# Optimization experiments

Hardware: AMD Instinct MI355X
Metric: run time of the kernel (lower is better)

Reference implementation:

```python
import jax, jax.numpy as jnp
import numpy as np

N_NODES = 50000
N_EDGES = 800000
D = 64          # node_in_feats == out_feats
N_STEPS = 3


def setup_inputs() -> dict:
    key = jax.random.key(0)
    ks = jax.random.split(key, 9)
    s = 1.0 / np.sqrt(D)
    return {
        "node_in": jax.random.normal(ks[0], (N_NODES, D), jnp.float32),
        # edge-type-0 linear (DGL GatedGraphConv self.linears[0])
        "W": jax.random.uniform(ks[1], (D, D), jnp.float32, -s, s),
        "b": jax.random.uniform(ks[2], (D,), jnp.float32, -s, s),
        # GRUCell params (torch layout: rows = [r, z, n] blocks)
        "Wih": jax.random.uniform(ks[3], (3 * D, D), jnp.float32, -s, s),
        "Whh": jax.random.uniform(ks[4], (3 * D, D), jnp.float32, -s, s),
        "bih": jax.random.uniform(ks[5], (3 * D,), jnp.float32, -s, s),
        "bhh": jax.random.uniform(ks[6], (3 * D,), jnp.float32, -s, s),
        "src": jax.random.randint(ks[7], (N_EDGES,), 0, N_NODES, jnp.int32),
        "dst": jax.random.randint(ks[8], (N_EDGES,), 0, N_NODES, jnp.int32),
    }


def _gru_cell(x, h, Wih, Whh, bih, bhh):
    gi = x @ Wih.T + bih   # [N, 3D]
    gh = h @ Whh.T + bhh   # [N, 3D]
    i_r, i_z, i_n = jnp.split(gi, 3, axis=-1)
    h_r, h_z, h_n = jnp.split(gh, 3, axis=-1)
    r = jax.nn.sigmoid(i_r + h_r)
    z = jax.nn.sigmoid(i_z + h_z)
    n = jnp.tanh(i_n + r * h_n)
    return (1.0 - z) * n + z * h


def reference(node_in, W, b, Wih, Whh, bih, bhh, src, dst):
    # DGL GatedGraphConv, n_steps=3, n_etypes=1. node_in_feats == out_feats,
    # so no zero-padding needed. The wrapper's tanh/dropout result is
    # discarded (h is overwritten by the second conv1 call), so the module
    # output is exactly one GatedGraphConv forward.
    h = node_in
    for _ in range(N_STEPS):
        wh = h @ W.T + b                                   # per-node transform; edge msg = wh[src]
        msg = wh[src]                                      # [E, D] gather
        a = jax.ops.segment_sum(msg, dst, num_segments=N_NODES)  # scatter-sum aggregation
        h = _gru_cell(a, h, Wih, Whh, bih, bhh)
    return h
```

## Files before the change

### kernel.cpp

```cpp
#include <hip/hip_runtime.h>

#define D 64
#define EXS 388
#define SGS 72
#define CHUNK 8192
#define PTH 512
#define MAXB 4096

typedef __bf16 bf16x8 __attribute__((ext_vector_type(8)));
typedef float f32x4 __attribute__((ext_vector_type(4)));

union U16 { uint4 u; bf16x8 b; };

__device__ __forceinline__ unsigned short f2bf(float f) {
    unsigned u = __float_as_uint(f);
    u += 0x7fff + ((u >> 16) & 1);
    return (unsigned short)(u >> 16);
}
__device__ __forceinline__ float bf2f(unsigned short s) {
    return __uint_as_float(((unsigned)s) << 16);
}


__global__ __launch_bounds__(256) void setup_kernel(const float* __restrict__ in,
                                                    unsigned short* __restrict__ hb0,
                                                    unsigned short* __restrict__ hb1,
                                                    const float* __restrict__ W,
                                                    const float* __restrict__ Wih,
                                                    const float* __restrict__ Whh,
                                                    const float* __restrict__ b,
                                                    unsigned short* __restrict__ Bpack,
                                                    float* __restrict__ cvec,
                                                    int* __restrict__ gcnt,
                                                    int n4, int nCvt, int N, int NBUK) {
    if ((int)blockIdx.x < nCvt) {
        int i = blockIdx.x * 256 + threadIdx.x;
        if (i < n4) {
            float4 v = ((const float4*)in)[i];
            ushort4 o;
            o.x = f2bf(v.x); o.y = f2bf(v.y); o.z = f2bf(v.z); o.w = f2bf(v.w);
            ((ushort4*)hb0)[i] = o;
        }
        if (blockIdx.x == 0) {
            if (threadIdx.x < 16) {
                ((ushort4*)(hb0 + (size_t)N * D))[threadIdx.x] = (ushort4){0, 0, 0, 0};
                ((ushort4*)(hb1 + (size_t)N * D))[threadIdx.x] = (ushort4){0, 0, 0, 0};
            }
            for (int j = threadIdx.x; j < NBUK; j += 256) gcnt[j] = 0;
        }
        return;
    }
    if (threadIdx.x >= 128) return;
    int blk = blockIdx.x - nCvt;
    int g = blk >> 2, t = blk & 3;
    int ks = threadIdx.x >> 6, lane = threadIdx.x & 63;
    int col = (g % 3) * 64 + t * 16 + (lane & 15);
    int kbase = ks * 32 + ((lane >> 4) & 3) * 8;
    size_t base = ((size_t)(blk * 2 + ks) * 64 + lane) * 8;
#pragma unroll
    for (int j = 0; j < 8; ++j) {
        int k = kbase + j;
        float v;
        if (g < 3) {
            v = 0.f;
#pragma unroll
            for (int m = 0; m < D; ++m) v += Wih[col * D + m] * W[m * D + k];
        } else {
            v = Whh[col * D + k];
        }
        Bpack[base + j] = f2bf(v);
    }
    if (g < 3 && ks == 0 && ((lane >> 4) & 3) == 0) {
        float acc = 0.f;
#pragma unroll
        for (int k = 0; k < D; ++k) acc += Wih[col * D + k] * b[k];
        cvec[col] = acc;
    }
}


__global__ __launch_bounds__(256) void count_kernel(const int* __restrict__ dst,
                                                    int* __restrict__ gcnt,
                                                    int E, int NBUK) {
    __shared__ int h[512];
    int g = blockIdx.x;
    for (int i = threadIdx.x; i < NBUK; i += 256) h[i] = 0;
    __syncthreads();
    int beg = g * CHUNK;
    int end = min(beg + CHUNK, E);
    for (int i = beg + threadIdx.x; i < end; i += 256)
        atomicAdd(&h[dst[i] >> 7], 1);
    __syncthreads();
    for (int i = threadIdx.x; i < NBUK; i += 256)
        if (h[i]) atomicAdd(&gcnt[i], h[i]);
}

__global__ __launch_bounds__(512) void bscan_kernel(const int* __restrict__ gcnt,
                                                    int* __restrict__ bucket_off,
                                                    int* __restrict__ gcursor,
                                                    int NBUK, int E) {
    __shared__ int scn[512];
    int t = threadIdx.x;
    int own = (t < NBUK) ? gcnt[t] : 0;
    scn[t] = own;
    __syncthreads();
    for (int off = 1; off < 512; off <<= 1) {
        int cur = scn[t];
        int add = (t >= off) ? scn[t - off] : 0;
        __syncthreads();
        scn[t] = cur + add;
        __syncthreads();
    }
    if (t < NBUK) {
        int excl = scn[t] - own;
        bucket_off[t] = excl;
        gcursor[t] = excl;
    }
    if (t == 0) bucket_off[NBUK] = E;
}

__global__ __launch_bounds__(PTH) void partition_kernel(const int* __restrict__ src,
                                                        const int* __restrict__ dst,
                                                        int* __restrict__ gcursor,
                                                        unsigned* __restrict__ pairs,
                                                        int E, int NBUK) {
    __shared__ unsigned pl[CHUNK];
    __shared__ unsigned short bk[CHUNK];
    __shared__ int hist[512];
    __shared__ int scn[512];
    __shared__ int goff[512];
    int g = blockIdx.x;
    int t = threadIdx.x;
    int beg = g * CHUNK;
    int end = min(beg + CHUNK, E);
    int m = end - beg;
    hist[t] = 0;
    __syncthreads();
    for (int i = t; i < m; i += PTH)
        atomicAdd(&hist[dst[beg + i] >> 7], 1);
    __syncthreads();
    int own = hist[t];
    scn[t] = own;
    __syncthreads();
    for (int off = 1; off < 512; off <<= 1) {
        int cur = scn[t];
        int add = (t >= off) ? scn[t - off] : 0;
        __syncthreads();
        scn[t] = cur + add;
        __syncthreads();
    }
    int excl = scn[t] - own;
    hist[t] = excl;
    if (t < NBUK) {
        int gbase = own ? atomicAdd(&gcursor[t], own) : 0;
        goff[t] = gbase - excl;
    }
    __syncthreads();
    for (int i = t; i < m; i += PTH) {
        int d = dst[beg + i];
        int s = src[beg + i];
        int b = d >> 7;
        int pos = atomicAdd(&hist[b], 1);
        pl[pos] = ((unsigned)s << 7) | (unsigned)(d & 127);
        bk[pos] = (unsigned short)b;
    }
    __syncthreads();
    for (int i = t; i < m; i += PTH)
        pairs[goff[bk[i]] + i] = pl[i];
}

__global__ __launch_bounds__(256) void bucket_sort_kernel(const unsigned* __restrict__ pairs,
                                                          const int* __restrict__ bucket_off,
                                                          int* __restrict__ srcs_sorted,
                                                          int* __restrict__ row_off,
                                                          int E, int NBUK, int N) {
    __shared__ unsigned pl[MAXB];
    __shared__ int srcl[MAXB];
    __shared__ int cnt[128];
    __shared__ int sc[128];
    __shared__ int cur2[128];
    int b = blockIdx.x;
    int t = threadIdx.x;
    int beg = bucket_off[b];
    int end = bucket_off[b + 1];
    int m = end - beg;
    if (m > MAXB) m = MAXB;
    if (t < 128) cnt[t] = 0;
    __syncthreads();
    for (int i = t; i < m; i += 256) {
        unsigned p = pairs[beg + i];
        pl[i] = p;
        atomicAdd(&cnt[p & 127], 1);
    }
    __syncthreads();
    int vt = 0;
    if (t < 128) { vt = cnt[t]; sc[t] = vt; }
    __syncthreads();
    for (int off = 1; off < 128; off <<= 1) {
        int v2 = 0;
        if (t < 128) { v2 = sc[t] + ((t >= off) ? sc[t - off] : 0); }
        __syncthreads();
        if (t < 128) sc[t] = v2;
        __syncthreads();
    }
    int excl = (t < 128) ? (sc[t] - vt) : 0;
    if (t < 128) {
        int gid = b * 128 + t;
        if (gid < N) row_off[gid] = beg + excl;
        cur2[t] = excl;
    }
    if (b == NBUK - 1 && t == 0) row_off[N] = E;
    __syncthreads();
    for (int i = t; i < m; i += 256) {
        unsigned p = pl[i];
        int r = atomicAdd(&cur2[p & 127], 1);
        srcl[r] = (int)(p >> 7);
    }
    __syncthreads();
    for (int i = t; i < m; i += 256) srcs_sorted[beg + i] = srcl[i];
}


__global__ __launch_bounds__(512) void fused2_kernel(const unsigned short* __restrict__ hb_in,
                                                     unsigned short* __restrict__ hb_out,
                                                     float* __restrict__ Fout, int writeF32,
                                                     const unsigned short* __restrict__ Bpack,
                                                     const float* __restrict__ cvec,
                                                     const float* __restrict__ bih,
                                                     const float* __restrict__ bhh,
                                                     const int* __restrict__ row_off,
                                                     const int* __restrict__ srcs,
                                                     int N) {
    __shared__ unsigned short sg[16 * SGS];
    __shared__ float ex[16 * EXS];
    int tid = threadIdx.x;
    int g = tid >> 6;
    int lane = tid & 63;
    int base = blockIdx.x * 16;

    {
        int es = lane >> 3;
        int fo = lane & 7;
        int nlA = g, nlB = g + 8;
        int nodeA = base + nlA, nodeB = base + nlB;
        int begA = 0, endA = 0, begB = 0, endB = 0;
        if (nodeA < N) { begA = row_off[nodeA]; endA = row_off[nodeA + 1]; }
        if (nodeB < N) { begB = row_off[nodeB]; endB = row_off[nodeB + 1]; }

        int sA[4], sB[4];
#pragma unroll
        for (int j = 0; j < 4; ++j) {
            int eA = begA + 8 * j + es;
            int eB = begB + 8 * j + es;
            sA[j] = (eA < endA) ? srcs[eA] : N;
            sB[j] = (eB < endB) ? srcs[eB] : N;
        }
        uint4 dA[4], dB[4];
#pragma unroll
        for (int j = 0; j < 4; ++j) dA[j] = *(const uint4*)(hb_in + (size_t)sA[j] * D + fo * 8);
#pragma unroll
        for (int j = 0; j < 4; ++j) dB[j] = *(const uint4*)(hb_in + (size_t)sB[j] * D + fo * 8);

        float accA[8], accB[8];
#pragma unroll
        for (int j = 0; j < 8; ++j) { accA[j] = 0.f; accB[j] = 0.f; }
#pragma unroll
        for (int j = 0; j < 4; ++j) {
            unsigned ua[4] = {dA[j].x, dA[j].y, dA[j].z, dA[j].w};
            unsigned ub[4] = {dB[j].x, dB[j].y, dB[j].z, dB[j].w};
#pragma unroll
            for (int k = 0; k < 4; ++k) {
                accA[2 * k]     += bf2f((unsigned short)(ua[k] & 0xffff));
                accA[2 * k + 1] += bf2f((unsigned short)(ua[k] >> 16));
                accB[2 * k]     += bf2f((unsigned short)(ub[k] & 0xffff));
                accB[2 * k + 1] += bf2f((unsigned short)(ub[k] >> 16));
            }
        }
        for (int i = begA + 32; i < endA; i += 8) {
            int e = i + es;
            int s = (e < endA) ? srcs[e] : N;
            uint4 dd = *(const uint4*)(hb_in + (size_t)s * D + fo * 8);
            unsigned uu[4] = {dd.x, dd.y, dd.z, dd.w};
#pragma unroll
            for (int k = 0; k < 4; ++k) {
                accA[2 * k]     += bf2f((unsigned short)(uu[k] & 0xffff));
                accA[2 * k + 1] += bf2f((unsigned short)(uu[k] >> 16));
            }
        }
        for (int i = begB + 32; i < endB; i += 8) {
            int e = i + es;
            int s = (e < endB) ? srcs[e] : N;
            uint4 dd = *(const uint4*)(hb_in + (size_t)s * D + fo * 8);
            unsigned uu[4] = {dd.x, dd.y, dd.z, dd.w};
#pragma unroll
            for (int k = 0; k < 4; ++k) {
                accB[2 * k]     += bf2f((unsigned short)(uu[k] & 0xffff));
                accB[2 * k + 1] += bf2f((unsigned short)(uu[k] >> 16));
            }
        }
#pragma unroll
        for (int st = 8; st < 64; st <<= 1)
#pragma unroll
            for (int j = 0; j < 8; ++j) {
                accA[j] += __shfl_xor(accA[j], st, 64);
                accB[j] += __shfl_xor(accB[j], st, 64);
            }
        if (es == 0) {
            uint4 oA, oB;
            oA.x = (unsigned)f2bf(accA[0]) | ((unsigned)f2bf(accA[1]) << 16);
            oA.y = (unsigned)f2bf(accA[2]) | ((unsigned)f2bf(accA[3]) << 16);
            oA.z = (unsigned)f2bf(accA[4]) | ((unsigned)f2bf(accA[5]) << 16);
            oA.w = (unsigned)f2bf(accA[6]) | ((unsigned)f2bf(accA[7]) << 16);
            oB.x = (unsigned)f2bf(accB[0]) | ((unsigned)f2bf(accB[1]) << 16);
            oB.y = (unsigned)f2bf(accB[2]) | ((unsigned)f2bf(accB[3]) << 16);
            oB.z = (unsigned)f2bf(accB[4]) | ((unsigned)f2bf(accB[5]) << 16);
            oB.w = (unsigned)f2bf(accB[6]) | ((unsigned)f2bf(accB[7]) << 16);
            *(uint4*)(sg + nlA * SGS + fo * 8) = oA;
            *(uint4*)(sg + nlB * SGS + fo * 8) = oB;
        }
    }
    __syncthreads();

    if (g < 6) {
        int r16 = lane & 15, quad = lane >> 4;
        bf16x8 bf[4][2];
        const uint4* bp = (const uint4*)Bpack;
#pragma unroll
        for (int t = 0; t < 4; ++t)
#pragma unroll
            for (int ks = 0; ks < 2; ++ks) {
                U16 u; u.u = bp[((g * 4 + t) * 2 + ks) * 64 + lane];
                bf[t][ks] = u.b;
            }
        bf16x8 af[2];
        if (g < 3) {
#pragma unroll
            for (int ks = 0; ks < 2; ++ks) {
                U16 u; u.u = *(const uint4*)(sg + r16 * SGS + ks * 32 + quad * 8);
                af[ks] = u.b;
            }
        } else {
            int row = base + r16;
            if (row >= N) row = N - 1;
#pragma unroll
            for (int ks = 0; ks < 2; ++ks) {
                U16 u; u.u = *(const uint4*)(hb_in + (size_t)row * D + ks * 32 + quad * 8);
                af[ks] = u.b;
            }
        }
        f32x4 acc[4];
#pragma unroll
        for (int t = 0; t < 4; ++t) acc[t] = (f32x4){0.f, 0.f, 0.f, 0.f};
#pragma unroll
        for (int t = 0; t < 4; ++t)
#pragma unroll
            for (int ks = 0; ks < 2; ++ks)
                acc[t] = __builtin_amdgcn_mfma_f32_16x16x32_bf16(af[ks], bf[t][ks], acc[t], 0, 0, 0);
#pragma unroll
        for (int t = 0; t < 4; ++t)
#pragma unroll
            for (int r = 0; r < 4; ++r)
                ex[(quad * 4 + r) * EXS + g * 64 + t * 16 + r16] = acc[t][r];
    }
    __syncthreads();

    for (int idx = tid; idx < 16 * D; idx += 512) {
        int i = idx >> 6, d = idx & 63;
        int node = base + i;
        if (node < N) {
            const float* p = &ex[i * EXS];
            float deg = (float)(row_off[node + 1] - row_off[node]);
            float ir = p[d] + bih[d] + deg * cvec[d];
            float iz = p[64 + d] + bih[64 + d] + deg * cvec[64 + d];
            float in_ = p[128 + d] + bih[128 + d] + deg * cvec[128 + d];
            float hr = p[192 + d] + bhh[d];
            float hz = p[256 + d] + bhh[64 + d];
            float hn = p[320 + d] + bhh[128 + d];
            float h = bf2f(hb_in[(size_t)node * D + d]);
            float r = 1.f / (1.f + __expf(-(ir + hr)));
            float z = 1.f / (1.f + __expf(-(iz + hz)));
            float nn = tanhf(in_ + r * hn);
            float hnew = (1.f - z) * nn + z * h;
            if (writeF32) Fout[(size_t)node * D + d] = hnew;
            else hb_out[(size_t)node * D + d] = f2bf(hnew);
        }
    }
}

extern "C" void kernel_launch(void* const* d_in, const int* in_sizes, int n_in,
                              void* d_out, int out_size, void* d_ws, size_t ws_size,
                              hipStream_t stream) {
    const float* node_in = (const float*)d_in[0];
    const float* W       = (const float*)d_in[1];
    const float* b       = (const float*)d_in[2];
    const float* Wih     = (const float*)d_in[3];
    const float* Whh     = (const float*)d_in[4];
    const float* bih     = (const float*)d_in[5];
    const float* bhh     = (const float*)d_in[6];
    const int*   src     = (const int*)d_in[7];
    const int*   dst     = (const int*)d_in[8];
    const int N = in_sizes[0] / D;
    const int E = in_sizes[7];
    float* out = (float*)d_out;

    const int G = (E + CHUNK - 1) / CHUNK;
    const int NBUK = (N + 127) >> 7;

    char* ws = (char*)d_ws;
    size_t off = 0;
    auto alloc = [&](size_t bytes) -> void* {
        void* p = ws + off;
        off += (bytes + 255) & ~(size_t)255;
        return p;
    };
    unsigned short* hb0    = (unsigned short*)alloc((size_t)(N + 1) * D * 2);
    unsigned short* hb1    = (unsigned short*)alloc((size_t)(N + 1) * D * 2);
    int*   row_off         = (int*)alloc((size_t)(N + 1) * sizeof(int));
    int*   srcs_sorted     = (int*)alloc((size_t)E * sizeof(int));
    unsigned* pairs        = (unsigned*)alloc((size_t)E * sizeof(unsigned));
    int*   gcnt            = (int*)alloc((size_t)NBUK * sizeof(int));
    int*   bucket_off      = (int*)alloc((size_t)(NBUK + 1) * sizeof(int));
    int*   gcursor         = (int*)alloc((size_t)NBUK * sizeof(int));
    unsigned short* Bpack  = (unsigned short*)alloc((size_t)6 * 4 * 2 * 64 * 8 * 2);
    float* cvec            = (float*)alloc((size_t)192 * sizeof(float));

    const int n4 = N * D / 4;
    const int nCvt = (n4 + 255) / 256;
    setup_kernel<<<nCvt + 24, 256, 0, stream>>>(node_in, hb0, hb1, W, Wih, Whh, b,
                                                Bpack, cvec, gcnt, n4, nCvt, N, NBUK);

    count_kernel<<<G, 256, 0, stream>>>(dst, gcnt, E, NBUK);
    bscan_kernel<<<1, 512, 0, stream>>>(gcnt, bucket_off, gcursor, NBUK, E);
    partition_kernel<<<G, PTH, 0, stream>>>(src, dst, gcursor, pairs, E, NBUK);
    bucket_sort_kernel<<<NBUK, 256, 0, stream>>>(pairs, bucket_off, srcs_sorted, row_off,
                                                 E, NBUK, N);

    const int grid = (N + 15) / 16;
    fused2_kernel<<<grid, 512, 0, stream>>>(hb0, hb1, out, 0, Bpack, cvec, bih, bhh,
                                            row_off, srcs_sorted, N);
    fused2_kernel<<<grid, 512, 0, stream>>>(hb1, hb0, out, 0, Bpack, cvec, bih, bhh,
                                            row_off, srcs_sorted, N);
    fused2_kernel<<<grid, 512, 0, stream>>>(hb0, hb1, out, 1, Bpack, cvec, bih, bhh,
                                            row_off, srcs_sorted, N);
}
```

Baseline: 222.6 us.

## Fold edge histogram into setup kernel and use per-chunk offsets; simplify gather loop

Merges the count kernel into the setup launch by writing a per-chunk bucket histogram matrix, which removes one launch and the global atomics. The scan kernel now computes per-chunk base offsets, so the partition step uses deterministic offsets instead of atomic cursors. The neighbor gather is rewritten into a helper that unrolls two rows at a time with explicit tail handling, replacing the fixed four-deep prefetch. The single-block scan now loops serially over all chunks, and the gather issues fewer loads in flight for low-degree nodes.

```diff
diff --git a/kernel.cpp b/kernel.cpp
--- a/kernel.cpp
+++ b/kernel.cpp
@@ -19,6 +19,44 @@
 }
 __device__ __forceinline__ float bf2f(unsigned short s) {
     return __uint_as_float(((unsigned)s) << 16);
+}
+
+__device__ __forceinline__ void addrow(float* acc, uint4 dd) {
+    unsigned uu[4] = {dd.x, dd.y, dd.z, dd.w};
+#pragma unroll
+    for (int k = 0; k < 4; ++k) {
+        acc[2 * k]     += bf2f((unsigned short)(uu[k] & 0xffff));
+        acc[2 * k + 1] += bf2f((unsigned short)(uu[k] >> 16));
+    }
+}
+
+__device__ __forceinline__ void gatherSum(float* acc, const int* __restrict__ srcs,
+                                          const unsigned short* __restrict__ hb,
+                                          int beg, int d, int es, int fo, int N) {
+    int full = d >> 3;
+    int rem  = d & 7;
+    int e = beg + es;
+    int j = 0;
+    for (; j + 2 <= full; j += 2) {
+        int s0 = srcs[e];
+        int s1 = srcs[e + 8];
+        uint4 d0 = *(const uint4*)(hb + (size_t)s0 * D + fo * 8);
+        uint4 d1 = *(const uint4*)(hb + (size_t)s1 * D + fo * 8);
+        addrow(acc, d0);
+        addrow(acc, d1);
+        e += 16;
+    }
+    if (j < full) {
+        int s0 = srcs[e];
+        uint4 d0 = *(const uint4*)(hb + (size_t)s0 * D + fo * 8);
+        addrow(acc, d0);
+        e += 8;
+    }
+    if (rem) {
+        int s0 = (es < rem) ? srcs[e] : N;
+        uint4 d0 = *(const uint4*)(hb + (size_t)s0 * D + fo * 8);
+        addrow(acc, d0);
+    }
 }
 
 
@@ -31,8 +69,10 @@
                                                     const float* __restrict__ b,
                                                     unsigned short* __restrict__ Bpack,
                                                     float* __restrict__ cvec,
-                                                    int* __restrict__ gcnt,
-                                                    int n4, int nCvt, int N, int NBUK) {
+                                                    const int* __restrict__ dst,
+                                                    int* __restrict__ Hmat,
+                                                    int n4, int nCvt, int N, int NBUK, int E) {
+    __shared__ int h[512];
     if ((int)blockIdx.x < nCvt) {
         int i = blockIdx.x * 256 + threadIdx.x;
         if (i < n4) {
@@ -41,17 +81,27 @@
             o.x = f2bf(v.x); o.y = f2bf(v.y); o.z = f2bf(v.z); o.w = f2bf(v.w);
             ((ushort4*)hb0)[i] = o;
         }
-        if (blockIdx.x == 0) {
-            if (threadIdx.x < 16) {
-                ((ushort4*)(hb0 + (size_t)N * D))[threadIdx.x] = (ushort4){0, 0, 0, 0};
-                ((ushort4*)(hb1 + (size_t)N * D))[threadIdx.x] = (ushort4){0, 0, 0, 0};
-            }
-            for (int j = threadIdx.x; j < NBUK; j += 256) gcnt[j] = 0;
+        if (blockIdx.x == 0 && threadIdx.x < 16) {
+            ((ushort4*)(hb0 + (size_t)N * D))[threadIdx.x] = (ushort4){0, 0, 0, 0};
+            ((ushort4*)(hb1 + (size_t)N * D))[threadIdx.x] = (ushort4){0, 0, 0, 0};
         }
         return;
     }
+    int blk = blockIdx.x - nCvt;
+    if (blk >= 24) {
+        int g = blk - 24;
+        for (int i = threadIdx.x; i < NBUK; i += 256) h[i] = 0;
+        __syncthreads();
+        int beg = g * CHUNK;
+        int end = min(beg + CHUNK, E);
+        for (int i = beg + threadIdx.x; i < end; i += 256)
+            atomicAdd(&h[dst[i] >> 7], 1);
+        __syncthreads();
+        for (int i = threadIdx.x; i < NBUK; i += 256)
+            Hmat[(size_t)g * NBUK + i] = h[i];
+        return;
+    }
     if (threadIdx.x >= 128) return;
-    int blk = blockIdx.x - nCvt;
     int g = blk >> 2, t = blk & 3;
     int ks = threadIdx.x >> 6, lane = threadIdx.x & 63;
     int col = (g % 3) * 64 + t * 16 + (lane & 15);
@@ -79,30 +129,20 @@
 }
 
 
-__global__ __launch_bounds__(256) void count_kernel(const int* __restrict__ dst,
-                                                    int* __restrict__ gcnt,
-                                                    int E, int NBUK) {
-    __shared__ int h[512];
-    int g = blockIdx.x;
-    for (int i = threadIdx.x; i < NBUK; i += 256) h[i] = 0;
-    __syncthreads();
-    int beg = g * CHUNK;
-    int end = min(beg + CHUNK, E);
-    for (int i = beg + threadIdx.x; i < end; i += 256)
-        atomicAdd(&h[dst[i] >> 7], 1);
-    __syncthreads();
-    for (int i = threadIdx.x; i < NBUK; i += 256)
-        if (h[i]) atomicAdd(&gcnt[i], h[i]);
-}
-
-__global__ __launch_bounds__(512) void bscan_kernel(const int* __restrict__ gcnt,
+__global__ __launch_bounds__(512) void bscan_kernel(const int* __restrict__ Hmat,
+                                                    int* __restrict__ chunk_base,
                                                     int* __restrict__ bucket_off,
-                                                    int* __restrict__ gcursor,
-                                                    int NBUK, int E) {
+                                                    int G, int NBUK, int E) {
     __shared__ int scn[512];
     int t = threadIdx.x;
-    int own = (t < NBUK) ? gcnt[t] : 0;
-    scn[t] = own;
+    int run = 0;
+    if (t < NBUK) {
+        for (int g = 0; g < G; ++g) {
+            chunk_base[(size_t)g * NBUK + t] = run;
+            run += Hmat[(size_t)g * NBUK + t];
+        }
+    }
+    scn[t] = (t < NBUK) ? run : 0;
     __syncthreads();
     for (int off = 1; off < 512; off <<= 1) {
         int cur = scn[t];
@@ -111,17 +151,14 @@
         scn[t] = cur + add;
         __syncthreads();
     }
-    if (t < NBUK) {
-        int excl = scn[t] - own;
-        bucket_off[t] = excl;
-        gcursor[t] = excl;
-    }
+    if (t < NBUK) bucket_off[t] = scn[t] - run;
     if (t == 0) bucket_off[NBUK] = E;
 }
 
 __global__ __launch_bounds__(PTH) void partition_kernel(const int* __restrict__ src,
                                                         const int* __restrict__ dst,
-                                                        int* __restrict__ gcursor,
+                                                        const int* __restrict__ chunk_base,
+                                                        const int* __restrict__ bucket_off,
                                                         unsigned* __restrict__ pairs,
                                                         int E, int NBUK) {
     __shared__ unsigned pl[CHUNK];
@@ -151,10 +188,8 @@
     }
     int excl = scn[t] - own;
     hist[t] = excl;
-    if (t < NBUK) {
-        int gbase = own ? atomicAdd(&gcursor[t], own) : 0;
-        goff[t] = gbase - excl;
-    }
+    if (t < NBUK)
+        goff[t] = bucket_off[t] + chunk_base[(size_t)g * NBUK + t] - excl;
     __syncthreads();
     for (int i = t; i < m; i += PTH) {
         int d = dst[beg + i];
@@ -241,63 +276,18 @@
     {
         int es = lane >> 3;
         int fo = lane & 7;
-        int nlA = g, nlB = g + 8;
-        int nodeA = base + nlA, nodeB = base + nlB;
+        int nodeA = base + g, nodeB = base + g + 8;
         int begA = 0, endA = 0, begB = 0, endB = 0;
         if (nodeA < N) { begA = row_off[nodeA]; endA = row_off[nodeA + 1]; }
         if (nodeB < N) { begB = row_off[nodeB]; endB = row_off[nodeB + 1]; }
 
-        int sA[4], sB[4];
-#pragma unroll
-        for (int j = 0; j < 4; ++j) {
-            int eA = begA + 8 * j + es;
-            int eB = begB + 8 * j + es;
-            sA[j] = (eA < endA) ? srcs[eA] : N;
-            sB[j] = (eB < endB) ? srcs[eB] : N;
-        }
-        uint4 dA[4], dB[4];
-#pragma unroll
-        for (int j = 0; j < 4; ++j) dA[j] = *(const uint4*)(hb_in + (size_t)sA[j] * D + fo * 8);
-#pragma unroll
-        for (int j = 0; j < 4; ++j) dB[j] = *(const uint4*)(hb_in + (size_t)sB[j] * D + fo * 8);
-
         float accA[8], accB[8];
 #pragma unroll
         for (int j = 0; j < 8; ++j) { accA[j] = 0.f; accB[j] = 0.f; }
-#pragma unroll
-        for (int j = 0; j < 4; ++j) {
-            unsigned ua[4] = {dA[j].x, dA[j].y, dA[j].z, dA[j].w};
-            unsigned ub[4] = {dB[j].x, dB[j].y, dB[j].z, dB[j].w};
-#pragma unroll
-            for (int k = 0; k < 4; ++k) {
-                accA[2 * k]     += bf2f((unsigned short)(ua[k] & 0xffff));
-                accA[2 * k + 1] += bf2f((unsigned short)(ua[k] >> 16));
-                accB[2 * k]     += bf2f((unsigned short)(ub[k] & 0xffff));
-                accB[2 * k + 1] += bf2f((unsigned short)(ub[k] >> 16));
-            }
-        }
-        for (int i = begA + 32; i < endA; i += 8) {
-            int e = i + es;
-            int s = (e < endA) ? srcs[e] : N;
-            uint4 dd = *(const uint4*)(hb_in + (size_t)s * D + fo * 8);
-            unsigned uu[4] = {dd.x, dd.y, dd.z, dd.w};
-#pragma unroll
-            for (int k = 0; k < 4; ++k) {
-                accA[2 * k]     += bf2f((unsigned short)(uu[k] & 0xffff));
-                accA[2 * k + 1] += bf2f((unsigned short)(uu[k] >> 16));
-            }
-        }
-        for (int i = begB + 32; i < endB; i += 8) {
-            int e = i + es;
-            int s = (e < endB) ? srcs[e] : N;
-            uint4 dd = *(const uint4*)(hb_in + (size_t)s * D + fo * 8);
-            unsigned uu[4] = {dd.x, dd.y, dd.z, dd.w};
-#pragma unroll
-            for (int k = 0; k < 4; ++k) {
-                accB[2 * k]     += bf2f((unsigned short)(uu[k] & 0xffff));
-                accB[2 * k + 1] += bf2f((unsigned short)(uu[k] >> 16));
-            }
-        }
+
+        gatherSum(accA, srcs, hb_in, begA, endA - begA, es, fo, N);
+        gatherSum(accB, srcs, hb_in, begB, endB - begB, es, fo, N);
+
 #pragma unroll
         for (int st = 8; st < 64; st <<= 1)
 #pragma unroll
@@ -315,8 +305,8 @@
             oB.y = (unsigned)f2bf(accB[2]) | ((unsigned)f2bf(accB[3]) << 16);
             oB.z = (unsigned)f2bf(accB[4]) | ((unsigned)f2bf(accB[5]) << 16);
             oB.w = (unsigned)f2bf(accB[6]) | ((unsigned)f2bf(accB[7]) << 16);
-            *(uint4*)(sg + nlA * SGS + fo * 8) = oA;
-            *(uint4*)(sg + nlB * SGS + fo * 8) = oB;
+            *(uint4*)(sg + g * SGS + fo * 8) = oA;
+            *(uint4*)(sg + (g + 8) * SGS + fo * 8) = oB;
         }
     }
     __syncthreads();
@@ -418,20 +408,20 @@
     int*   row_off         = (int*)alloc((size_t)(N + 1) * sizeof(int));
     int*   srcs_sorted     = (int*)alloc((size_t)E * sizeof(int));
     unsigned* pairs        = (unsigned*)alloc((size_t)E * sizeof(unsigned));
-    int*   gcnt            = (int*)alloc((size_t)NBUK * sizeof(int));
     int*   bucket_off      = (int*)alloc((size_t)(NBUK + 1) * sizeof(int));
-    int*   gcursor         = (int*)alloc((size_t)NBUK * sizeof(int));
+    int*   Hmat            = (int*)alloc((size_t)G * NBUK * sizeof(int));
+    int*   chunk_base      = (int*)alloc((size_t)G * NBUK * sizeof(int));
     unsigned short* Bpack  = (unsigned short*)alloc((size_t)6 * 4 * 2 * 64 * 8 * 2);
     float* cvec            = (float*)alloc((size_t)192 * sizeof(float));
 
     const int n4 = N * D / 4;
     const int nCvt = (n4 + 255) / 256;
-    setup_kernel<<<nCvt + 24, 256, 0, stream>>>(node_in, hb0, hb1, W, Wih, Whh, b,
-                                                Bpack, cvec, gcnt, n4, nCvt, N, NBUK);
-
-    count_kernel<<<G, 256, 0, stream>>>(dst, gcnt, E, NBUK);
-    bscan_kernel<<<1, 512, 0, stream>>>(gcnt, bucket_off, gcursor, NBUK, E);
-    partition_kernel<<<G, PTH, 0, stream>>>(src, dst, gcursor, pairs, E, NBUK);
+    setup_kernel<<<nCvt + 24 + G, 256, 0, stream>>>(node_in, hb0, hb1, W, Wih, Whh, b,
+                                                    Bpack, cvec, dst, Hmat,
+                                                    n4, nCvt, N, NBUK, E);
+
+    bscan_kernel<<<1, 512, 0, stream>>>(Hmat, chunk_base, bucket_off, G, NBUK, E);
+    partition_kernel<<<G, PTH, 0, stream>>>(src, dst, chunk_base, bucket_off, pairs, E, NBUK);
     bucket_sort_kernel<<<NBUK, 256, 0, stream>>>(pairs, bucket_off, srcs_sorted, row_off,
                                                  E, NBUK, N);
 
```

Measured after the change: 253.3 us. +13.8%, slower.

## Use fixed-capacity bucket slots to drop count and scan kernels

Applied to the files above, without the earlier changes.

Replaces the exact prefix-sum bucket layout with fixed MAXB-sized slots per destination bucket. The partition kernel's atomic cursor then gives both the offset and the final count, so the separate count and scan kernels, and their extra pass over dst, are removed. Rows are described by separate begin/end arrays instead of a CSR offset array. In exchange, buckets holding more than MAXB edges would be silently truncated, and the pairs and sorted-source buffers become padded and larger.

```diff
diff --git a/kernel.cpp b/kernel.cpp
--- a/kernel.cpp
+++ b/kernel.cpp
@@ -31,7 +31,7 @@
                                                     const float* __restrict__ b,
                                                     unsigned short* __restrict__ Bpack,
                                                     float* __restrict__ cvec,
-                                                    int* __restrict__ gcnt,
+                                                    int* __restrict__ gcursor,
                                                     int n4, int nCvt, int N, int NBUK) {
     if ((int)blockIdx.x < nCvt) {
         int i = blockIdx.x * 256 + threadIdx.x;
@@ -46,7 +46,7 @@
                 ((ushort4*)(hb0 + (size_t)N * D))[threadIdx.x] = (ushort4){0, 0, 0, 0};
                 ((ushort4*)(hb1 + (size_t)N * D))[threadIdx.x] = (ushort4){0, 0, 0, 0};
             }
-            for (int j = threadIdx.x; j < NBUK; j += 256) gcnt[j] = 0;
+            for (int j = threadIdx.x; j < NBUK; j += 256) gcursor[j] = 0;
         }
         return;
     }
@@ -78,46 +78,6 @@
     }
 }
 
-
-__global__ __launch_bounds__(256) void count_kernel(const int* __restrict__ dst,
-                                                    int* __restrict__ gcnt,
-                                                    int E, int NBUK) {
-    __shared__ int h[512];
-    int g = blockIdx.x;
-    for (int i = threadIdx.x; i < NBUK; i += 256) h[i] = 0;
-    __syncthreads();
-    int beg = g * CHUNK;
-    int end = min(beg + CHUNK, E);
-    for (int i = beg + threadIdx.x; i < end; i += 256)
-        atomicAdd(&h[dst[i] >> 7], 1);
-    __syncthreads();
-    for (int i = threadIdx.x; i < NBUK; i += 256)
-        if (h[i]) atomicAdd(&gcnt[i], h[i]);
-}
-
-__global__ __launch_bounds__(512) void bscan_kernel(const int* __restrict__ gcnt,
-                                                    int* __restrict__ bucket_off,
-                                                    int* __restrict__ gcursor,
-                                                    int NBUK, int E) {
-    __shared__ int scn[512];
-    int t = threadIdx.x;
-    int own = (t < NBUK) ? gcnt[t] : 0;
-    scn[t] = own;
-    __syncthreads();
-    for (int off = 1; off < 512; off <<= 1) {
-        int cur = scn[t];
-        int add = (t >= off) ? scn[t - off] : 0;
-        __syncthreads();
-        scn[t] = cur + add;
-        __syncthreads();
-    }
-    if (t < NBUK) {
-        int excl = scn[t] - own;
-        bucket_off[t] = excl;
-        gcursor[t] = excl;
-    }
-    if (t == 0) bucket_off[NBUK] = E;
-}
 
 __global__ __launch_bounds__(PTH) void partition_kernel(const int* __restrict__ src,
                                                         const int* __restrict__ dst,
@@ -153,7 +113,7 @@
     hist[t] = excl;
     if (t < NBUK) {
         int gbase = own ? atomicAdd(&gcursor[t], own) : 0;
-        goff[t] = gbase - excl;
+        goff[t] = t * MAXB + gbase - excl;
     }
     __syncthreads();
     for (int i = t; i < m; i += PTH) {
@@ -169,11 +129,13 @@
         pairs[goff[bk[i]] + i] = pl[i];
 }
 
+
 __global__ __launch_bounds__(256) void bucket_sort_kernel(const unsigned* __restrict__ pairs,
-                                                          const int* __restrict__ bucket_off,
+                                                          const int* __restrict__ gcnt,
                                                           int* __restrict__ srcs_sorted,
-                                                          int* __restrict__ row_off,
-                                                          int E, int NBUK, int N) {
+                                                          int* __restrict__ row_beg,
+                                                          int* __restrict__ row_end,
+                                                          int NBUK, int N) {
     __shared__ unsigned pl[MAXB];
     __shared__ int srcl[MAXB];
     __shared__ int cnt[128];
@@ -181,9 +143,8 @@
     __shared__ int cur2[128];
     int b = blockIdx.x;
     int t = threadIdx.x;
-    int beg = bucket_off[b];
-    int end = bucket_off[b + 1];
-    int m = end - beg;
+    int beg = b * MAXB;
+    int m = gcnt[b];
     if (m > MAXB) m = MAXB;
     if (t < 128) cnt[t] = 0;
     __syncthreads();
@@ -206,10 +167,12 @@
     int excl = (t < 128) ? (sc[t] - vt) : 0;
     if (t < 128) {
         int gid = b * 128 + t;
-        if (gid < N) row_off[gid] = beg + excl;
+        if (gid < N) {
+            row_beg[gid] = beg + excl;
+            row_end[gid] = beg + excl + vt;
+        }
         cur2[t] = excl;
     }
-    if (b == NBUK - 1 && t == 0) row_off[N] = E;
     __syncthreads();
     for (int i = t; i < m; i += 256) {
         unsigned p = pl[i];
@@ -228,7 +191,8 @@
                                                      const float* __restrict__ cvec,
                                                      const float* __restrict__ bih,
                                                      const float* __restrict__ bhh,
-                                                     const int* __restrict__ row_off,
+                                                     const int* __restrict__ row_beg,
+                                                     const int* __restrict__ row_end,
                                                      const int* __restrict__ srcs,
                                                      int N) {
     __shared__ unsigned short sg[16 * SGS];
@@ -244,8 +208,8 @@
         int nlA = g, nlB = g + 8;
         int nodeA = base + nlA, nodeB = base + nlB;
         int begA = 0, endA = 0, begB = 0, endB = 0;
-        if (nodeA < N) { begA = row_off[nodeA]; endA = row_off[nodeA + 1]; }
-        if (nodeB < N) { begB = row_off[nodeB]; endB = row_off[nodeB + 1]; }
+        if (nodeA < N) { begA = row_beg[nodeA]; endA = row_end[nodeA]; }
+        if (nodeB < N) { begB = row_beg[nodeB]; endB = row_end[nodeB]; }
 
         int sA[4], sB[4];
 #pragma unroll
@@ -369,7 +333,7 @@
         int node = base + i;
         if (node < N) {
             const float* p = &ex[i * EXS];
-            float deg = (float)(row_off[node + 1] - row_off[node]);
+            float deg = (float)(row_end[node] - row_beg[node]);
             float ir = p[d] + bih[d] + deg * cvec[d];
             float iz = p[64 + d] + bih[64 + d] + deg * cvec[64 + d];
             float in_ = p[128 + d] + bih[128 + d] + deg * cvec[128 + d];
@@ -415,11 +379,10 @@
     };
     unsigned short* hb0    = (unsigned short*)alloc((size_t)(N + 1) * D * 2);
     unsigned short* hb1    = (unsigned short*)alloc((size_t)(N + 1) * D * 2);
-    int*   row_off         = (int*)alloc((size_t)(N + 1) * sizeof(int));
-    int*   srcs_sorted     = (int*)alloc((size_t)E * sizeof(int));
-    unsigned* pairs        = (unsigned*)alloc((size_t)E * sizeof(unsigned));
-    int*   gcnt            = (int*)alloc((size_t)NBUK * sizeof(int));
-    int*   bucket_off      = (int*)alloc((size_t)(NBUK + 1) * sizeof(int));
+    int*   row_beg         = (int*)alloc((size_t)NBUK * 128 * sizeof(int));
+    int*   row_end         = (int*)alloc((size_t)NBUK * 128 * sizeof(int));
+    int*   srcs_sorted     = (int*)alloc((size_t)NBUK * MAXB * sizeof(int));
+    unsigned* pairs        = (unsigned*)alloc((size_t)NBUK * MAXB * sizeof(unsigned));
     int*   gcursor         = (int*)alloc((size_t)NBUK * sizeof(int));
     unsigned short* Bpack  = (unsigned short*)alloc((size_t)6 * 4 * 2 * 64 * 8 * 2);
     float* cvec            = (float*)alloc((size_t)192 * sizeof(float));
@@ -427,19 +390,17 @@
     const int n4 = N * D / 4;
     const int nCvt = (n4 + 255) / 256;
     setup_kernel<<<nCvt + 24, 256, 0, stream>>>(node_in, hb0, hb1, W, Wih, Whh, b,
-                                                Bpack, cvec, gcnt, n4, nCvt, N, NBUK);
-
-    count_kernel<<<G, 256, 0, stream>>>(dst, gcnt, E, NBUK);
-    bscan_kernel<<<1, 512, 0, stream>>>(gcnt, bucket_off, gcursor, NBUK, E);
+                                                Bpack, cvec, gcursor, n4, nCvt, N, NBUK);
+
     partition_kernel<<<G, PTH, 0, stream>>>(src, dst, gcursor, pairs, E, NBUK);
-    bucket_sort_kernel<<<NBUK, 256, 0, stream>>>(pairs, bucket_off, srcs_sorted, row_off,
-                                                 E, NBUK, N);
+    bucket_sort_kernel<<<NBUK, 256, 0, stream>>>(pairs, gcursor, srcs_sorted,
+                                                 row_beg, row_end, NBUK, N);
 
     const int grid = (N + 15) / 16;
     fused2_kernel<<<grid, 512, 0, stream>>>(hb0, hb1, out, 0, Bpack, cvec, bih, bhh,
-                                            row_off, srcs_sorted, N);
+                                            row_beg, row_end, srcs_sorted, N);
     fused2_kernel<<<grid, 512, 0, stream>>>(hb1, hb0, out, 0, Bpack, cvec, bih, bhh,
-                                            row_off, srcs_sorted, N);
+                                            row_beg, row_end, srcs_sorted, N);
     fused2_kernel<<<grid, 512, 0, stream>>>(hb0, hb1, out, 1, Bpack, cvec, bih, bhh,
-                                            row_off, srcs_sorted, N);
-}
+                                            row_beg, row_end, srcs_sorted, N);
+}
```

Measured after the change: 207.7 us. -6.7%, faster.
